# Performance work log

Hardware: AMD Instinct MI355X
Metric: run time of the kernel (lower is better)

## Reference

```python
import jax, jax.numpy as jnp
import numpy as np

N = 4096  # input_features == output_features == transform length (power of 2)


def _fft(x, twiddle_factors):
    """Faithful vectorized form of the module's radix-2 butterfly network.

    x: (N, D) complex64. twiddle_factors: (N, D) float32 (the learned weights).
    Original loop: for each stage `step`, for each block, for r in [0, half):
        k = r * (N // step)
        temp = exp(-2j*pi*k/N * twiddle_factors[k]) * x[j + half]
        new x[j + half] = x[j] - temp ; new x[j] = x[j] + temp
    Blocks are independent, so each stage is a single batched butterfly.
    """
    n = x.shape[0]
    # initial permutation: index xor with N//2 (as written in the source; not full bit-reversal)
    x = x[jnp.bitwise_xor(jnp.arange(n), n // 2)]
    step = 2
    while step <= n:  # log2(N) stages, fixed small Python loop
        half = step // 2
        k = jnp.arange(half) * (n // step)                      # (half,)
        phase = (-2.0 * jnp.pi) * (k[:, None].astype(jnp.float32) / n) * twiddle_factors[k]
        tw = jnp.exp(1j * phase)                                # (half, D) complex64
        xr = x.reshape(n // step, step, -1)                     # (blocks, step, D)
        top = xr[:, :half]
        bot = xr[:, half:]
        temp = tw[None] * bot                                   # (blocks, half, D)
        x = jnp.concatenate([top + temp, top - temp], axis=1).reshape(n, -1)
        step *= 2
    return x


def setup_inputs() -> dict:
    key = jax.random.key(0)
    kx, kw = jax.random.split(key)
    x = jax.random.normal(kx, (N, N), dtype=jnp.float32)
    weights = jax.random.normal(kw, (N, N), dtype=jnp.float32)  # nn.Parameter(randn(out, in))
    return {"x": x, "weights": weights}


def reference(x, weights):
    # input_features == output_features -> no pad / no truncation branch taken
    return _fft(x.astype(jnp.complex64), weights)
```

## Files before the change

### kernel.cpp

```cpp
#include <hip/hip_runtime.h>

#define NEG_TWOPI -6.28318530717958647692f

__device__ __forceinline__ void bf(float& ar, float& ai, float& br, float& bi,
                                   float s, float cs) {
    float tr = cs * br - s * bi;
    float ti = cs * bi + s * br;
    br = ar - tr; bi = ai - ti;
    ar = ar + tr; ai = ai + ti;
}

__global__ __launch_bounds__(256) void fft_lo(const float* __restrict__ x,
                                              const float* __restrict__ w,
                                              float4* __restrict__ dst4,
                                              unsigned dst_lim4) {
    __shared__ __align__(16) float2 tile[64 * 64];
    const int t  = threadIdx.x;
    const int c0 = (blockIdx.x & 63) << 6;
    const int r0 = (blockIdx.x >> 6) << 6;
    const int src_r0 = r0 ^ 2048;

    const float4* x4    = (const float4*)x;
    float4*       tile4 = (float4*)tile;
#pragma unroll
    for (int l = 0; l < 4; ++l) {
        int idx = l * 256 + t;
        int row = idx >> 4;
        int cg  = idx & 15;
        float4 v = x4[(size_t)(src_r0 + row) * 1024 + (c0 >> 2) + cg];
        tile4[(row << 5) + (cg << 1) + 0] = make_float4(v.x, 0.f, v.y, 0.f);
        tile4[(row << 5) + (cg << 1) + 1] = make_float4(v.z, 0.f, v.w, 0.f);
    }
    __syncthreads();

    const int c  = t & 63;
    const int pb = t >> 6;

    float ar[16], ai[16];
#pragma unroll
    for (int m = 0; m < 16; ++m) {
        float2 v = tile[(16 * pb + m) * 64 + c];
        ar[m] = v.x; ai[m] = v.y;
    }

#pragma unroll
    for (int h = 1; h <= 8; h <<= 1) {
        const int step = h << 1;
        const int kmul = 4096 / step;
#pragma unroll
        for (int r = 0; r < h; ++r) {
            float s = 0.f, cs = 1.f;
            if (r != 0) {
                const int k = r * kmul;
                const float wk = w[(size_t)k * 4096 + c0 + c];
                __sincosf(NEG_TWOPI * ((float)k * (1.f / 4096.f)) * wk, &s, &cs);
            }
#pragma unroll
            for (int b = 0; b < 8 / h; ++b) {
                const int mt = b * step + r;
                bf(ar[mt], ai[mt], ar[mt + h], ai[mt + h], s, cs);
            }
        }
    }

#pragma unroll
    for (int m = 0; m < 16; ++m)
        tile[(16 * pb + m) * 64 + c] = make_float2(ar[m], ai[m]);
    __syncthreads();
#pragma unroll
    for (int m = 0; m < 16; ++m) {
        float2 v = tile[(pb + 4 * m) * 64 + c];
        ar[m] = v.x; ai[m] = v.y;
    }

#pragma unroll
    for (int rm = 0; rm < 4; ++rm) {
        const int j = pb + 4 * rm;
        const int k = j * 128;
        float s, cs;
        const float wk = w[(size_t)k * 4096 + c0 + c];
        __sincosf(NEG_TWOPI * ((float)k * (1.f / 4096.f)) * wk, &s, &cs);
#pragma unroll
        for (int b = 0; b < 2; ++b) {
            const int mt = b * 8 + rm;
            bf(ar[mt], ai[mt], ar[mt + 4], ai[mt + 4], s, cs);
        }
    }
#pragma unroll
    for (int m = 0; m < 8; ++m) {
        const int j = pb + 4 * m;
        const int k = j * 64;
        float s, cs;
        const float wk = w[(size_t)k * 4096 + c0 + c];
        __sincosf(NEG_TWOPI * ((float)k * (1.f / 4096.f)) * wk, &s, &cs);
        bf(ar[m], ai[m], ar[m + 8], ai[m + 8], s, cs);
    }

#pragma unroll
    for (int m = 0; m < 16; ++m)
        tile[(pb + 4 * m) * 64 + c] = make_float2(ar[m], ai[m]);
    __syncthreads();
#pragma unroll
    for (int l = 0; l < 8; ++l) {
        int idx = l * 256 + t;
        int row = idx >> 5;
        int cp  = idx & 31;
        size_t gi = (size_t)(r0 + row) * 2048 + (c0 >> 1) + cp;
        if (gi < dst_lim4) dst4[gi] = tile4[(row << 5) + cp];
    }
}

template <int REAL_OUT>
__global__ __launch_bounds__(256) void fft_hi(const float* __restrict__ w,
                                              const float4* __restrict__ src4,
                                              float4* __restrict__ dst4,
                                              unsigned src_lim4,
                                              unsigned dst_lim4) {
    __shared__ __align__(16) float2 tile[64 * 64];
    const int t    = threadIdx.x;
    const int c0   = (blockIdx.x & 63) << 6;
    const int rres = blockIdx.x >> 6;

    float4* tile4 = (float4*)tile;
#pragma unroll
    for (int l = 0; l < 8; ++l) {
        int idx = l * 256 + t;
        int j   = idx >> 5;
        int cp  = idx & 31;
        size_t gi = (size_t)(rres + (j << 6)) * 2048 + (c0 >> 1) + cp;
        tile4[(j << 5) + cp] = (gi < src_lim4) ? src4[gi]
                                               : make_float4(0.f, 0.f, 0.f, 0.f);
    }
    __syncthreads();

    const int c  = t & 63;
    const int pb = t >> 6;

    float ar[16], ai[16];
#pragma unroll
    for (int m = 0; m < 16; ++m) {
        float2 v = tile[(16 * pb + m) * 64 + c];
        ar[m] = v.x; ai[m] = v.y;
    }

#pragma unroll
    for (int h = 1; h <= 8; h <<= 1) {
        const int step = h << 1;
        const int kmul = 32 / h;
#pragma unroll
        for (int r = 0; r < h; ++r) {
            const int k = (rres + 64 * r) * kmul;
            float s, cs;
            const float wk = w[(size_t)k * 4096 + c0 + c];
            __sincosf(NEG_TWOPI * ((float)k * (1.f / 4096.f)) * wk, &s, &cs);
#pragma unroll
            for (int b = 0; b < 8 / h; ++b) {
                const int mt = b * step + r;
                bf(ar[mt], ai[mt], ar[mt + h], ai[mt + h], s, cs);
            }
        }
    }

#pragma unroll
    for (int m = 0; m < 16; ++m)
        tile[(16 * pb + m) * 64 + c] = make_float2(ar[m], ai[m]);
    __syncthreads();
#pragma unroll
    for (int m = 0; m < 16; ++m) {
        float2 v = tile[(pb + 4 * m) * 64 + c];
        ar[m] = v.x; ai[m] = v.y;
    }

#pragma unroll
    for (int rm = 0; rm < 4; ++rm) {
        const int j = pb + 4 * rm;
        const int k = (rres + 64 * j) * 2;
        float s, cs;
        const float wk = w[(size_t)k * 4096 + c0 + c];
        __sincosf(NEG_TWOPI * ((float)k * (1.f / 4096.f)) * wk, &s, &cs);
#pragma unroll
        for (int b = 0; b < 2; ++b) {
            const int mt = b * 8 + rm;
            bf(ar[mt], ai[mt], ar[mt + 4], ai[mt + 4], s, cs);
        }
    }
#pragma unroll
    for (int m = 0; m < 8; ++m) {
        const int j = pb + 4 * m;
        const int k = rres + 64 * j;
        float s, cs;
        const float wk = w[(size_t)k * 4096 + c0 + c];
        __sincosf(NEG_TWOPI * ((float)k * (1.f / 4096.f)) * wk, &s, &cs);
        bf(ar[m], ai[m], ar[m + 8], ai[m + 8], s, cs);
    }

#pragma unroll
    for (int m = 0; m < 16; ++m)
        tile[(pb + 4 * m) * 64 + c] = make_float2(ar[m], ai[m]);
    __syncthreads();

    if (REAL_OUT) {
#pragma unroll
        for (int l = 0; l < 4; ++l) {
            int idx = l * 256 + t;
            int j   = idx >> 4;
            int g   = idx & 15;
            float4 v;
            v.x = tile[(j << 6) + 4 * g + 0].x;
            v.y = tile[(j << 6) + 4 * g + 1].x;
            v.z = tile[(j << 6) + 4 * g + 2].x;
            v.w = tile[(j << 6) + 4 * g + 3].x;
            size_t gi = (size_t)(rres + (j << 6)) * 1024 + (c0 >> 2) + g;
            if (gi < dst_lim4) dst4[gi] = v;
        }
    } else {
#pragma unroll
        for (int l = 0; l < 8; ++l) {
            int idx = l * 256 + t;
            int j   = idx >> 5;
            int cp  = idx & 31;
            size_t gi = (size_t)(rres + (j << 6)) * 2048 + (c0 >> 1) + cp;
            if (gi < dst_lim4) dst4[gi] = tile4[(j << 5) + cp];
        }
    }
}

extern "C" void kernel_launch(void* const* d_in, const int* in_sizes, int n_in,
                              void* d_out, int out_size, void* d_ws, size_t ws_size,
                              hipStream_t stream) {
    const float* x = (const float*)d_in[0];
    const float* w = (const float*)d_in[1];
    const long long NN = 4096LL * 4096LL;

    if ((long long)out_size >= 2 * NN) {
        float4* o4 = (float4*)d_out;
        unsigned lim4 = (unsigned)(out_size / 4);
        fft_lo<<<4096, 256, 0, stream>>>(x, w, o4, lim4);
        fft_hi<0><<<4096, 256, 0, stream>>>(w, o4, o4, lim4, lim4);
    } else {
        float4* ws4 = (float4*)d_ws;
        unsigned ws_lim4  = (unsigned)(ws_size / 16);
        unsigned out_lim4 = (unsigned)(out_size / 4);
        fft_lo<<<4096, 256, 0, stream>>>(x, w, ws4, ws_lim4);
        fft_hi<1><<<4096, 256, 0, stream>>>(w, (const float4*)ws4, (float4*)d_out,
                                            ws_lim4, out_lim4);
    }
}
```

Baseline: 219.2 us.

## Load and store FFT data directly from global memory, prefetch twiddle weights early

Both kernels drop the shared-memory staging used for the initial global load and the final store. Each thread now reads its column elements straight from global memory and writes its results straight back, which leaves one shared-memory transpose per kernel instead of three. All twiddle weight loads are issued up front and the sincos values are computed before they are needed, so memory latency can overlap with compute. The cost is narrower per-thread accesses (scalar float or float2 instead of float4) and higher register pressure. In the real-output path only the real part is written, as scalar stores.

```diff
diff --git a/kernel.cpp b/kernel.cpp
--- a/kernel.cpp
+++ b/kernel.cpp
@@ -1,6 +1,7 @@
 #include <hip/hip_runtime.h>
 
 #define NEG_TWOPI -6.28318530717958647692f
+#define INV_N (1.0f / 4096.0f)
 
 __device__ __forceinline__ void bf(float& ar, float& ai, float& br, float& bi,
                                    float s, float cs) {
@@ -10,51 +11,55 @@
     ar = ar + tr; ai = ai + ti;
 }
 
+__device__ __forceinline__ void tw(int k, float wk, float* s, float* cs) {
+    __sincosf(NEG_TWOPI * ((float)k * INV_N) * wk, s, cs);
+}
+
 __global__ __launch_bounds__(256) void fft_lo(const float* __restrict__ x,
                                               const float* __restrict__ w,
-                                              float4* __restrict__ dst4,
-                                              unsigned dst_lim4) {
+                                              float2* __restrict__ dst2,
+                                              unsigned dst_lim2) {
     __shared__ __align__(16) float2 tile[64 * 64];
-    const int t  = threadIdx.x;
-    const int c0 = (blockIdx.x & 63) << 6;
-    const int r0 = (blockIdx.x >> 6) << 6;
+    const int t   = threadIdx.x;
+    const int c   = t & 63;
+    const int pb  = t >> 6;
+    const int c0  = (blockIdx.x & 63) << 6;
+    const int r0  = (blockIdx.x >> 6) << 6;
     const int src_r0 = r0 ^ 2048;
-
-    const float4* x4    = (const float4*)x;
-    float4*       tile4 = (float4*)tile;
-#pragma unroll
-    for (int l = 0; l < 4; ++l) {
-        int idx = l * 256 + t;
-        int row = idx >> 4;
-        int cg  = idx & 15;
-        float4 v = x4[(size_t)(src_r0 + row) * 1024 + (c0 >> 2) + cg];
-        tile4[(row << 5) + (cg << 1) + 0] = make_float4(v.x, 0.f, v.y, 0.f);
-        tile4[(row << 5) + (cg << 1) + 1] = make_float4(v.z, 0.f, v.w, 0.f);
-    }
-    __syncthreads();
-
-    const int c  = t & 63;
-    const int pb = t >> 6;
+    const int col = c0 + c;
+
+    float wp1[7];
+#pragma unroll
+    for (int i = 0; i < 7; ++i)
+        wp1[i] = w[(size_t)(256 * (i + 1)) * 4096 + col];
+    float w2a[4], w2b[8];
+#pragma unroll
+    for (int i = 0; i < 4; ++i)
+        w2a[i] = w[(size_t)((pb + 4 * i) * 128) * 4096 + col];
+#pragma unroll
+    for (int i = 0; i < 8; ++i)
+        w2b[i] = w[(size_t)((pb + 4 * i) * 64) * 4096 + col];
 
     float ar[16], ai[16];
 #pragma unroll
     for (int m = 0; m < 16; ++m) {
-        float2 v = tile[(16 * pb + m) * 64 + c];
-        ar[m] = v.x; ai[m] = v.y;
-    }
+        ar[m] = x[(size_t)(src_r0 + 16 * pb + m) * 4096 + col];
+        ai[m] = 0.f;
+    }
+
+    float s1[8], c1[8];
+    s1[0] = 0.f; c1[0] = 1.f;
+#pragma unroll
+    for (int i = 1; i < 8; ++i)
+        tw(256 * i, wp1[i - 1], &s1[i], &c1[i]);
 
 #pragma unroll
     for (int h = 1; h <= 8; h <<= 1) {
         const int step = h << 1;
-        const int kmul = 4096 / step;
 #pragma unroll
         for (int r = 0; r < h; ++r) {
-            float s = 0.f, cs = 1.f;
-            if (r != 0) {
-                const int k = r * kmul;
-                const float wk = w[(size_t)k * 4096 + c0 + c];
-                __sincosf(NEG_TWOPI * ((float)k * (1.f / 4096.f)) * wk, &s, &cs);
-            }
+            const int ti = r * (8 / h);
+            const float s = s1[ti], cs = c1[ti];
 #pragma unroll
             for (int b = 0; b < 8 / h; ++b) {
                 const int mt = b * step + r;
@@ -63,6 +68,14 @@
         }
     }
 
+    float s2a[4], c2a[4], s2b[8], c2b[8];
+#pragma unroll
+    for (int i = 0; i < 4; ++i)
+        tw((pb + 4 * i) * 128, w2a[i], &s2a[i], &c2a[i]);
+#pragma unroll
+    for (int i = 0; i < 8; ++i)
+        tw((pb + 4 * i) * 64, w2b[i], &s2b[i], &c2b[i]);
+
 #pragma unroll
     for (int m = 0; m < 16; ++m)
         tile[(16 * pb + m) * 64 + c] = make_float2(ar[m], ai[m]);
@@ -75,91 +88,104 @@
 
 #pragma unroll
     for (int rm = 0; rm < 4; ++rm) {
-        const int j = pb + 4 * rm;
-        const int k = j * 128;
-        float s, cs;
-        const float wk = w[(size_t)k * 4096 + c0 + c];
-        __sincosf(NEG_TWOPI * ((float)k * (1.f / 4096.f)) * wk, &s, &cs);
 #pragma unroll
         for (int b = 0; b < 2; ++b) {
             const int mt = b * 8 + rm;
-            bf(ar[mt], ai[mt], ar[mt + 4], ai[mt + 4], s, cs);
-        }
-    }
-#pragma unroll
-    for (int m = 0; m < 8; ++m) {
-        const int j = pb + 4 * m;
-        const int k = j * 64;
-        float s, cs;
-        const float wk = w[(size_t)k * 4096 + c0 + c];
-        __sincosf(NEG_TWOPI * ((float)k * (1.f / 4096.f)) * wk, &s, &cs);
-        bf(ar[m], ai[m], ar[m + 8], ai[m + 8], s, cs);
-    }
-
-#pragma unroll
-    for (int m = 0; m < 16; ++m)
-        tile[(pb + 4 * m) * 64 + c] = make_float2(ar[m], ai[m]);
-    __syncthreads();
-#pragma unroll
-    for (int l = 0; l < 8; ++l) {
-        int idx = l * 256 + t;
-        int row = idx >> 5;
-        int cp  = idx & 31;
-        size_t gi = (size_t)(r0 + row) * 2048 + (c0 >> 1) + cp;
-        if (gi < dst_lim4) dst4[gi] = tile4[(row << 5) + cp];
+            bf(ar[mt], ai[mt], ar[mt + 4], ai[mt + 4], s2a[rm], c2a[rm]);
+        }
+    }
+#pragma unroll
+    for (int m = 0; m < 8; ++m)
+        bf(ar[m], ai[m], ar[m + 8], ai[m + 8], s2b[m], c2b[m]);
+
+#pragma unroll
+    for (int m = 0; m < 16; ++m) {
+        size_t gi = (size_t)(r0 + pb + 4 * m) * 4096 + col;
+        if (gi < dst_lim2) dst2[gi] = make_float2(ar[m], ai[m]);
     }
 }
 
 template <int REAL_OUT>
 __global__ __launch_bounds__(256) void fft_hi(const float* __restrict__ w,
-                                              const float4* __restrict__ src4,
-                                              float4* __restrict__ dst4,
-                                              unsigned src_lim4,
-                                              unsigned dst_lim4) {
+                                              const float2* __restrict__ src2,
+                                              float2* __restrict__ dstc,
+                                              float* __restrict__ dstr,
+                                              unsigned dst_lim) {
     __shared__ __align__(16) float2 tile[64 * 64];
     const int t    = threadIdx.x;
+    const int c    = t & 63;
+    const int pb   = t >> 6;
     const int c0   = (blockIdx.x & 63) << 6;
     const int rres = blockIdx.x >> 6;
-
-    float4* tile4 = (float4*)tile;
-#pragma unroll
-    for (int l = 0; l < 8; ++l) {
-        int idx = l * 256 + t;
-        int j   = idx >> 5;
-        int cp  = idx & 31;
-        size_t gi = (size_t)(rres + (j << 6)) * 2048 + (c0 >> 1) + cp;
-        tile4[(j << 5) + cp] = (gi < src_lim4) ? src4[gi]
-                                               : make_float4(0.f, 0.f, 0.f, 0.f);
-    }
-    __syncthreads();
-
-    const int c  = t & 63;
-    const int pb = t >> 6;
+    const int col  = c0 + c;
+
+    float wp1, wp2[2], wp4[4], wp8[8];
+    wp1 = w[(size_t)(rres * 32) * 4096 + col];
+#pragma unroll
+    for (int r = 0; r < 2; ++r)
+        wp2[r] = w[(size_t)((rres + 64 * r) * 16) * 4096 + col];
+#pragma unroll
+    for (int r = 0; r < 4; ++r)
+        wp4[r] = w[(size_t)((rres + 64 * r) * 8) * 4096 + col];
+#pragma unroll
+    for (int r = 0; r < 8; ++r)
+        wp8[r] = w[(size_t)((rres + 64 * r) * 4) * 4096 + col];
+    float w2a[4], w2b[8];
+#pragma unroll
+    for (int i = 0; i < 4; ++i)
+        w2a[i] = w[(size_t)((rres + 64 * (pb + 4 * i)) * 2) * 4096 + col];
+#pragma unroll
+    for (int i = 0; i < 8; ++i)
+        w2b[i] = w[(size_t)(rres + 64 * (pb + 4 * i)) * 4096 + col];
 
     float ar[16], ai[16];
 #pragma unroll
     for (int m = 0; m < 16; ++m) {
-        float2 v = tile[(16 * pb + m) * 64 + c];
+        float2 v = src2[(size_t)(rres + 64 * (16 * pb + m)) * 4096 + col];
         ar[m] = v.x; ai[m] = v.y;
     }
 
-#pragma unroll
-    for (int h = 1; h <= 8; h <<= 1) {
-        const int step = h << 1;
-        const int kmul = 32 / h;
-#pragma unroll
-        for (int r = 0; r < h; ++r) {
-            const int k = (rres + 64 * r) * kmul;
-            float s, cs;
-            const float wk = w[(size_t)k * 4096 + c0 + c];
-            __sincosf(NEG_TWOPI * ((float)k * (1.f / 4096.f)) * wk, &s, &cs);
-#pragma unroll
-            for (int b = 0; b < 8 / h; ++b) {
-                const int mt = b * step + r;
-                bf(ar[mt], ai[mt], ar[mt + h], ai[mt + h], s, cs);
-            }
-        }
-    }
+    {
+        float s, cs;
+        tw(rres * 32, wp1, &s, &cs);
+#pragma unroll
+        for (int b = 0; b < 8; ++b)
+            bf(ar[2 * b], ai[2 * b], ar[2 * b + 1], ai[2 * b + 1], s, cs);
+    }
+#pragma unroll
+    for (int r = 0; r < 2; ++r) {
+        float s, cs;
+        tw((rres + 64 * r) * 16, wp2[r], &s, &cs);
+#pragma unroll
+        for (int b = 0; b < 4; ++b) {
+            const int mt = b * 4 + r;
+            bf(ar[mt], ai[mt], ar[mt + 2], ai[mt + 2], s, cs);
+        }
+    }
+#pragma unroll
+    for (int r = 0; r < 4; ++r) {
+        float s, cs;
+        tw((rres + 64 * r) * 8, wp4[r], &s, &cs);
+#pragma unroll
+        for (int b = 0; b < 2; ++b) {
+            const int mt = b * 8 + r;
+            bf(ar[mt], ai[mt], ar[mt + 4], ai[mt + 4], s, cs);
+        }
+    }
+#pragma unroll
+    for (int r = 0; r < 8; ++r) {
+        float s, cs;
+        tw((rres + 64 * r) * 4, wp8[r], &s, &cs);
+        bf(ar[r], ai[r], ar[r + 8], ai[r + 8], s, cs);
+    }
+
+    float s2a[4], c2a[4], s2b[8], c2b[8];
+#pragma unroll
+    for (int i = 0; i < 4; ++i)
+        tw((rres + 64 * (pb + 4 * i)) * 2, w2a[i], &s2a[i], &c2a[i]);
+#pragma unroll
+    for (int i = 0; i < 8; ++i)
+        tw(rres + 64 * (pb + 4 * i), w2b[i], &s2b[i], &c2b[i]);
 
 #pragma unroll
     for (int m = 0; m < 16; ++m)
@@ -173,54 +199,27 @@
 
 #pragma unroll
     for (int rm = 0; rm < 4; ++rm) {
-        const int j = pb + 4 * rm;
-        const int k = (rres + 64 * j) * 2;
-        float s, cs;
-        const float wk = w[(size_t)k * 4096 + c0 + c];
-        __sincosf(NEG_TWOPI * ((float)k * (1.f / 4096.f)) * wk, &s, &cs);
 #pragma unroll
         for (int b = 0; b < 2; ++b) {
             const int mt = b * 8 + rm;
-            bf(ar[mt], ai[mt], ar[mt + 4], ai[mt + 4], s, cs);
-        }
-    }
-#pragma unroll
-    for (int m = 0; m < 8; ++m) {
-        const int j = pb + 4 * m;
-        const int k = rres + 64 * j;
-        float s, cs;
-        const float wk = w[(size_t)k * 4096 + c0 + c];
-        __sincosf(NEG_TWOPI * ((float)k * (1.f / 4096.f)) * wk, &s, &cs);
-        bf(ar[m], ai[m], ar[m + 8], ai[m + 8], s, cs);
-    }
-
-#pragma unroll
-    for (int m = 0; m < 16; ++m)
-        tile[(pb + 4 * m) * 64 + c] = make_float2(ar[m], ai[m]);
-    __syncthreads();
+            bf(ar[mt], ai[mt], ar[mt + 4], ai[mt + 4], s2a[rm], c2a[rm]);
+        }
+    }
+#pragma unroll
+    for (int m = 0; m < 8; ++m)
+        bf(ar[m], ai[m], ar[m + 8], ai[m + 8], s2b[m], c2b[m]);
 
     if (REAL_OUT) {
 #pragma unroll
-        for (int l = 0; l < 4; ++l) {
-            int idx = l * 256 + t;
-            int j   = idx >> 4;
-            int g   = idx & 15;
-            float4 v;
-            v.x = tile[(j << 6) + 4 * g + 0].x;
-            v.y = tile[(j << 6) + 4 * g + 1].x;
-            v.z = tile[(j << 6) + 4 * g + 2].x;
-            v.w = tile[(j << 6) + 4 * g + 3].x;
-            size_t gi = (size_t)(rres + (j << 6)) * 1024 + (c0 >> 2) + g;
-            if (gi < dst_lim4) dst4[gi] = v;
+        for (int m = 0; m < 16; ++m) {
+            size_t gi = (size_t)(rres + 64 * (pb + 4 * m)) * 4096 + col;
+            if (gi < dst_lim) dstr[gi] = ar[m];
         }
     } else {
 #pragma unroll
-        for (int l = 0; l < 8; ++l) {
-            int idx = l * 256 + t;
-            int j   = idx >> 5;
-            int cp  = idx & 31;
-            size_t gi = (size_t)(rres + (j << 6)) * 2048 + (c0 >> 1) + cp;
-            if (gi < dst_lim4) dst4[gi] = tile4[(j << 5) + cp];
+        for (int m = 0; m < 16; ++m) {
+            size_t gi = (size_t)(rres + 64 * (pb + 4 * m)) * 4096 + col;
+            if (gi < dst_lim) dstc[gi] = make_float2(ar[m], ai[m]);
         }
     }
 }
@@ -233,16 +232,16 @@
     const long long NN = 4096LL * 4096LL;
 
     if ((long long)out_size >= 2 * NN) {
-        float4* o4 = (float4*)d_out;
-        unsigned lim4 = (unsigned)(out_size / 4);
-        fft_lo<<<4096, 256, 0, stream>>>(x, w, o4, lim4);
-        fft_hi<0><<<4096, 256, 0, stream>>>(w, o4, o4, lim4, lim4);
+        float2* o2 = (float2*)d_out;
+        unsigned lim2 = (unsigned)(out_size / 2);
+        fft_lo<<<4096, 256, 0, stream>>>(x, w, o2, lim2);
+        fft_hi<0><<<4096, 256, 0, stream>>>(w, o2, o2, nullptr, lim2);
     } else {
-        float4* ws4 = (float4*)d_ws;
-        unsigned ws_lim4  = (unsigned)(ws_size / 16);
-        unsigned out_lim4 = (unsigned)(out_size / 4);
-        fft_lo<<<4096, 256, 0, stream>>>(x, w, ws4, ws_lim4);
-        fft_hi<1><<<4096, 256, 0, stream>>>(w, (const float4*)ws4, (float4*)d_out,
-                                            ws_lim4, out_lim4);
-    }
-}
+        float2* ws2 = (float2*)d_ws;
+        unsigned ws_lim2 = (unsigned)(ws_size / 8);
+        unsigned out_lim = (unsigned)out_size;
+        fft_lo<<<4096, 256, 0, stream>>>(x, w, ws2, ws_lim2);
+        fft_hi<1><<<4096, 256, 0, stream>>>(w, (const float2*)ws2, nullptr,
+                                            (float*)d_out, out_lim);
+    }
+}
```

Result: faster. 211.3 us (-3.6%).
